# Kernel tuning notes

Hardware: AMD Instinct MI355X
Metric: run time of the kernel (lower is better)

## Reference

```python
import jax, jax.numpy as jnp
import numpy as np

D = 1024      # model_dim (input_dim)
H = 2048      # hidden_size_per_expert (hardcoded in module)
E = 8         # num_experts
K = 2         # topk
T = 8192      # tokens (batch after view)


def setup_inputs() -> dict:
    key = jax.random.key(0)
    ks = jax.random.split(key, 6)
    s_in = 1.0 / np.sqrt(D)
    s_h = 1.0 / np.sqrt(H)
    return {
        "x": jax.random.normal(ks[0], (T, D), dtype=jnp.float32),
        "wg": jax.random.normal(ks[1], (D, E), dtype=jnp.float32) * s_in,   # gate Linear(D,E,bias=False)
        "w1": jax.random.normal(ks[2], (E, D, H), dtype=jnp.float32) * s_in,
        "b1": jnp.zeros((E, H), dtype=jnp.float32),
        "w2": jax.random.normal(ks[3], (E, H, D), dtype=jnp.float32) * s_h,
        "b2": jnp.zeros((E, D), dtype=jnp.float32),
    }


def _moe(x, wg, w1, b1, w2, b2):
    # top-k gating (Tutel 'top' gate, k=K)
    logits = x @ wg                         # [T,E]
    scores = jax.nn.softmax(logits, -1)     # [T,E]
    topv, topi = jax.lax.top_k(scores, K)   # [T,K]
    sel = jax.nn.one_hot(topi, E, dtype=x.dtype)          # [T,K,E]
    combine = jnp.einsum('tk,tke->te', topv, sel)          # sparse combine weights [T,E]
    # GShard-style load-balance aux loss (top-1 dispatch mask)
    ce = sel[:, 0, :].mean(0)               # fraction of tokens whose top1 is e
    me = scores.mean(0)                     # mean gate prob per expert
    l_aux = jnp.sum(me * ce) * E
    # expert FFN (dense over experts; combine zeros out non-selected)
    h = jax.nn.relu(jnp.einsum('td,edh->teh', x, w1) + b1)  # [T,E,H]
    y = jnp.einsum('teh,ehd->ted', h, w2) + b2              # [T,E,D]
    out = jnp.einsum('te,ted->td', combine, y)              # [T,D]
    return out, l_aux


def reference(x, wg, w1, b1, w2, b2):
    return _moe(x, wg, w1, b1, w2, b2)
```

## Files before the change

kernel.cpp:

```cpp
#include <hip/hip_runtime.h>
#include <stdint.h>

#define T_TOK 8192
#define DIM   1024
#define HID   2048
#define NE    8

#define BM 256
#define BN 256
#define BK 64

#define GB_TOK 32

typedef float floatx4 __attribute__((ext_vector_type(4)));
typedef short shortx8 __attribute__((ext_vector_type(8)));

typedef __attribute__((address_space(3))) void       lds_void;
typedef const __attribute__((address_space(1))) void gbl_void;

__device__ __forceinline__ unsigned short f2bf(float f) {
  unsigned int u = __float_as_uint(f);
  unsigned int r = 0x7fffu + ((u >> 16) & 1u);
  return (unsigned short)((u + r) >> 16);
}

__global__ __launch_bounds__(256) void transpose_cast_kernel(const float* __restrict__ in,
                                                             unsigned short* __restrict__ out,
                                                             int R, int C) {
  __shared__ float tile[32][33];
  const size_t eoff = (size_t)blockIdx.z * R * C;
  const float* ip = in + eoff;
  unsigned short* op = out + eoff;
  int c0 = blockIdx.x * 32, r0 = blockIdx.y * 32;
  int tx = threadIdx.x, ty = threadIdx.y;
#pragma unroll
  for (int i = 0; i < 4; i++)
    tile[ty + i * 8][tx] = ip[(size_t)(r0 + ty + i * 8) * C + (c0 + tx)];
  __syncthreads();
#pragma unroll
  for (int i = 0; i < 4; i++)
    op[(size_t)(c0 + ty + i * 8) * R + (r0 + tx)] = f2bf(tile[tx][ty + i * 8]);
}

__global__ __launch_bounds__(256) void gate_kernel(const float* __restrict__ x,
                                                   const float* __restrict__ wg,
                                                   unsigned short* __restrict__ xb,
                                                   int* counts, int* top1cnt, float* ssum,
                                                   int* tok_list, float* wgt_list) {
  __shared__ int   lds_cnt[8];
  __shared__ int   lds_top1[8];
  __shared__ float lds_ssum[4][8];
  __shared__ int   tk_e[GB_TOK][2];
  __shared__ int   tk_r[GB_TOK][2];
  __shared__ float tk_w[GB_TOK][2];
  __shared__ int   base[8];

  const int tid = threadIdx.x;
  const int wave = tid >> 6;
  const int lane = tid & 63;

  if (tid < 8) { lds_cnt[tid] = 0; lds_top1[tid] = 0; }
  if (tid < 32) lds_ssum[tid >> 3][tid & 7] = 0.f;
  __syncthreads();

  float ssum_local[8];
#pragma unroll
  for (int e = 0; e < 8; e++) ssum_local[e] = 0.f;

  for (int it = 0; it < GB_TOK / 4; it++) {
    const int lt = it * 4 + wave;
    const int t = blockIdx.x * GB_TOK + lt;

    float acc[8];
#pragma unroll
    for (int e = 0; e < 8; e++) acc[e] = 0.f;
    const float* xr = x + (size_t)t * DIM;
    unsigned short* xw = xb + (size_t)t * DIM;
#pragma unroll
    for (int i = 0; i < 16; i++) {
      int d = i * 64 + lane;
      float xv = xr[d];
      xw[d] = f2bf(xv);
      const float4* wr = reinterpret_cast<const float4*>(wg + d * 8);
      float4 w0 = wr[0], w1 = wr[1];
      acc[0] += xv * w0.x; acc[1] += xv * w0.y; acc[2] += xv * w0.z; acc[3] += xv * w0.w;
      acc[4] += xv * w1.x; acc[5] += xv * w1.y; acc[6] += xv * w1.z; acc[7] += xv * w1.w;
    }
#pragma unroll
    for (int e = 0; e < 8; e++) {
#pragma unroll
      for (int off = 32; off > 0; off >>= 1) acc[e] += __shfl_xor(acc[e], off, 64);
    }
    if (lane == 0) {
      float mx = acc[0];
#pragma unroll
      for (int e = 1; e < 8; e++) mx = fmaxf(mx, acc[e]);
      float s[8], sum = 0.f;
#pragma unroll
      for (int e = 0; e < 8; e++) { s[e] = expf(acc[e] - mx); sum += s[e]; }
      float inv = 1.f / sum;
#pragma unroll
      for (int e = 0; e < 8; e++) { s[e] *= inv; ssum_local[e] += s[e]; }
      int i1 = 0;
#pragma unroll
      for (int e = 1; e < 8; e++) if (s[e] > s[i1]) i1 = e;
      int i2 = (i1 == 0) ? 1 : 0;
#pragma unroll
      for (int e = 0; e < 8; e++) if (e != i1 && s[e] > s[i2]) i2 = e;
      atomicAdd(&lds_top1[i1], 1);
      int r1 = atomicAdd(&lds_cnt[i1], 1);
      int r2 = atomicAdd(&lds_cnt[i2], 1);
      tk_e[lt][0] = i1; tk_r[lt][0] = r1; tk_w[lt][0] = s[i1];
      tk_e[lt][1] = i2; tk_r[lt][1] = r2; tk_w[lt][1] = s[i2];
    }
  }
  if (lane == 0) {
#pragma unroll
    for (int e = 0; e < 8; e++) lds_ssum[wave][e] = ssum_local[e];
  }
  __syncthreads();
  if (tid < 8) {
    base[tid] = atomicAdd(&counts[tid], lds_cnt[tid]);
    atomicAdd(&top1cnt[tid], lds_top1[tid]);
    atomicAdd(&ssum[tid],
              lds_ssum[0][tid] + lds_ssum[1][tid] + lds_ssum[2][tid] + lds_ssum[3][tid]);
  }
  __syncthreads();
  if (tid < GB_TOK * 2) {
    int lt = tid >> 1, k = tid & 1;
    int e = tk_e[lt][k];
    int pos = base[e] + tk_r[lt][k];
    tok_list[e * T_TOK + pos] = blockIdx.x * GB_TOK + lt;
    wgt_list[e * T_TOK + pos] = tk_w[lt][k];
  }
}

__global__ void scan_kernel(const int* counts, const int* top1cnt, const float* ssum,
                            int* h_off, float* laux_out) {
  if (threadIdx.x == 0 && blockIdx.x == 0) {
    int off = 0;
    float l = 0.f;
    for (int e = 0; e < 8; e++) {
      h_off[e] = off;
      off += counts[e];
      l += (ssum[e] / (float)T_TOK) * ((float)top1cnt[e] / (float)T_TOK);
    }
    *laux_out = l * (float)NE;
  }
}

template <int MODE>
__global__ __launch_bounds__(512, 2) void moe_gemm_kernel(
    const unsigned short* __restrict__ A_src, const unsigned short* __restrict__ B_src,
    const float* __restrict__ bias, const int* __restrict__ counts,
    const int* __restrict__ h_off, const int* __restrict__ tok_list,
    const float* __restrict__ wgt_list, unsigned short* __restrict__ h_out,
    float* __restrict__ out, int N, int K) {
  __shared__ unsigned short s_a[2][BM][BK];
  __shared__ unsigned short s_b[2][BN][BK];

  const int e = blockIdx.z;
  const int n_e = counts[e];
  const int m0 = blockIdx.y * BM;
  if (m0 >= n_e) return;
  const int n0 = blockIdx.x * BN;
  const int tid = threadIdx.x;

  const int lane = tid & 63;
  const int wv = tid >> 6;
  const int lrow = lane >> 3;
  const int lchk = (lane & 7) ^ lrow;

  const unsigned short* a_g[4];
  const unsigned short* b_g[4];
#pragma unroll
  for (int c = 0; c < 4; c++) {
    int ra = c * 64 + wv * 8 + lrow;
    int gr = m0 + ra;
    int safe = (gr < n_e) ? gr : (n_e - 1);
    const unsigned short* abase;
    if (MODE == 0) {
      int tok = tok_list[e * T_TOK + safe];
      abase = A_src + (size_t)tok * K;
    } else {
      abase = A_src + (size_t)(h_off[e] + safe) * K;
    }
    a_g[c] = abase + lchk * 8;
    b_g[c] = B_src + ((size_t)e * N + n0 + ra) * K + lchk * 8;
  }

  auto STAGE = [&](int buf, int kt) {
#pragma unroll
    for (int c = 0; c < 4; c++) {
      __builtin_amdgcn_global_load_lds((gbl_void*)(a_g[c] + kt),
                                       (lds_void*)&s_a[buf][c * 64 + wv * 8][0], 16, 0, 0);
      __builtin_amdgcn_global_load_lds((gbl_void*)(b_g[c] + kt),
                                       (lds_void*)&s_b[buf][c * 64 + wv * 8][0], 16, 0, 0);
    }
  };

  const int lm = lane & 15;
  const int quad = lane >> 4;
  const int r7 = lm & 7;
  const int wm = (wv >> 2) * 128;
  const int wn = (wv & 3) * 64;

  floatx4 acc[8][4];
#pragma unroll
  for (int mi = 0; mi < 8; mi++)
#pragma unroll
    for (int ni = 0; ni < 4; ni++) acc[mi][ni] = (floatx4){0.f, 0.f, 0.f, 0.f};

  const int NT = K / BK;
  STAGE(0, 0);
  __syncthreads();

  int cur = 0;
  for (int t = 0; t < NT; ++t) {
    if (t + 1 < NT) STAGE(cur ^ 1, (t + 1) * BK);
#pragma unroll
    for (int kk = 0; kk < 2; kk++) {
      const int pc = ((kk << 2) + quad) ^ r7;
      shortx8 af[8], bfr[4];
#pragma unroll
      for (int mi = 0; mi < 8; mi++)
        af[mi] = *reinterpret_cast<const shortx8*>(&s_a[cur][wm + mi * 16 + lm][pc << 3]);
#pragma unroll
      for (int ni = 0; ni < 4; ni++)
        bfr[ni] = *reinterpret_cast<const shortx8*>(&s_b[cur][wn + ni * 16 + lm][pc << 3]);
#pragma unroll
      for (int mi = 0; mi < 8; mi++)
#pragma unroll
        for (int ni = 0; ni < 4; ni++)
          acc[mi][ni] = __builtin_amdgcn_mfma_f32_16x16x32_bf16(af[mi], bfr[ni], acc[mi][ni], 0, 0, 0);
    }
    __syncthreads();
    cur ^= 1;
  }

#pragma unroll
  for (int mi = 0; mi < 8; mi++) {
#pragma unroll
    for (int r = 0; r < 4; r++) {
      int row = m0 + wm + mi * 16 + quad * 4 + r;
      if (row >= n_e) continue;
      if (MODE == 0) {
        size_t base = (size_t)(h_off[e] + row) * N;
#pragma unroll
        for (int ni = 0; ni < 4; ni++) {
          int col = n0 + wn + ni * 16 + lm;
          float v = acc[mi][ni][r] + bias[e * N + col];
          v = fmaxf(v, 0.f);
          h_out[base + col] = f2bf(v);
        }
      } else {
        int tok = tok_list[e * T_TOK + row];
        float wgt = wgt_list[e * T_TOK + row];
        size_t base = (size_t)tok * N;
#pragma unroll
        for (int ni = 0; ni < 4; ni++) {
          int col = n0 + wn + ni * 16 + lm;
          float v = wgt * (acc[mi][ni][r] + bias[e * N + col]);
          atomicAdd(&out[base + col], v);
        }
      }
    }
  }
}

extern "C" void kernel_launch(void* const* d_in, const int* in_sizes, int n_in,
                              void* d_out, int out_size, void* d_ws, size_t ws_size,
                              hipStream_t stream) {
  const float* x  = (const float*)d_in[0];
  const float* wg = (const float*)d_in[1];
  const float* w1 = (const float*)d_in[2];
  const float* b1 = (const float*)d_in[3];
  const float* w2 = (const float*)d_in[4];
  const float* b2 = (const float*)d_in[5];
  float* out = (float*)d_out;

  char* ws = (char*)d_ws;
  int*            counts   = (int*)(ws + 0);
  int*            top1cnt  = (int*)(ws + 32);
  float*          ssum     = (float*)(ws + 64);
  int*            h_off    = (int*)(ws + 96);
  int*            tok_list = (int*)(ws + 256);
  float*          wgt_list = (float*)(ws + 262400);
  unsigned short* x_bf     = (unsigned short*)(ws + 524544);
  unsigned short* w1t      = (unsigned short*)(ws + 17301760);
  unsigned short* w2t      = (unsigned short*)(ws + 50856192);
  unsigned short* h_buf    = (unsigned short*)(ws + 84410624);

  hipMemsetAsync(ws, 0, 256, stream);
  hipMemsetAsync(d_out, 0, (size_t)out_size * sizeof(float), stream);

  dim3 tb(32, 8);
  transpose_cast_kernel<<<dim3(HID / 32, DIM / 32, NE), tb, 0, stream>>>(w1, w1t, DIM, HID);
  transpose_cast_kernel<<<dim3(DIM / 32, HID / 32, NE), tb, 0, stream>>>(w2, w2t, HID, DIM);

  gate_kernel<<<T_TOK / GB_TOK, 256, 0, stream>>>(x, wg, x_bf, counts, top1cnt, ssum,
                                                  tok_list, wgt_list);
  scan_kernel<<<1, 64, 0, stream>>>(counts, top1cnt, ssum, h_off, out + (size_t)T_TOK * DIM);

  moe_gemm_kernel<0><<<dim3(HID / BN, T_TOK / BM, NE), 512, 0, stream>>>(
      x_bf, w1t, b1, counts, h_off, tok_list, wgt_list, h_buf, nullptr, HID, DIM);
  moe_gemm_kernel<1><<<dim3(DIM / BN, T_TOK / BM, NE), 512, 0, stream>>>(
      h_buf, w2t, b2, counts, h_off, tok_list, wgt_list, nullptr, out, DIM, HID);
}
```

Measured before the change: 574.0 us.

## Compact expert tile grid and software-pipeline MoE GEMM with split-K LDS stages

Replaces the per-expert 3D grid, which launched many empty blocks, with a compact 1D tile index built from prefix offsets computed in the scan kernel, so only real tiles are launched (at most 72). The GEMM main loop is rewritten as an explicit 8-phase pipeline: the LDS tile is split into two 32-wide K halves and two 128-row halves, and global-to-LDS loads are interleaved with MFMA groups using fine-grained barriers, vmcnt waits and setprio. A new XOR swizzle layout is used for the LDS reads. This trades simpler code for hand-scheduled synchronisation that depends on exact vmcnt accounting, and the fixed grid size of 72 assumes the tile count never exceeds it.

```diff
diff --git a/kernel.cpp b/kernel.cpp
--- a/kernel.cpp
+++ b/kernel.cpp
@@ -136,74 +136,125 @@
 }
 
 __global__ void scan_kernel(const int* counts, const int* top1cnt, const float* ssum,
-                            int* h_off, float* laux_out) {
+                            int* h_off, int* tile_off, float* laux_out) {
   if (threadIdx.x == 0 && blockIdx.x == 0) {
-    int off = 0;
+    int off = 0, toff = 0;
     float l = 0.f;
     for (int e = 0; e < 8; e++) {
       h_off[e] = off;
+      tile_off[e] = toff;
       off += counts[e];
+      toff += (counts[e] + BM - 1) / BM;
       l += (ssum[e] / (float)T_TOK) * ((float)top1cnt[e] / (float)T_TOK);
     }
+    tile_off[8] = toff;
     *laux_out = l * (float)NE;
   }
 }
+
+
+#define LDA4(buf, kk, mh)                                                        \
+  do {                                                                           \
+    const char* ha_ = (const char*)&s_a[buf][kk][0][0];                          \
+    _Pragma("unroll") for (int j_ = 0; j_ < 4; j_++)                             \
+        af[j_] = *reinterpret_cast<const shortx8*>(ha_ + aoff + ((mh)*4 + j_) * 1024); \
+  } while (0)
+
+#define LDB4(buf, kk)                                                            \
+  do {                                                                           \
+    const char* hb_ = (const char*)&s_b[buf][kk][0][0];                          \
+    _Pragma("unroll") for (int j_ = 0; j_ < 4; j_++)                             \
+        bfr[j_] = *reinterpret_cast<const shortx8*>(hb_ + boff + j_ * 1024);     \
+  } while (0)
+
+#define MFMA16(mh)                                                               \
+  do {                                                                           \
+    __builtin_amdgcn_s_setprio(1);                                               \
+    _Pragma("unroll") for (int j_ = 0; j_ < 4; j_++)                             \
+        _Pragma("unroll") for (int n_ = 0; n_ < 4; n_++)                         \
+            acc[(mh)*4 + j_][n_] = __builtin_amdgcn_mfma_f32_16x16x32_bf16(      \
+                af[j_], bfr[n_], acc[(mh)*4 + j_][n_], 0, 0, 0);                 \
+    __builtin_amdgcn_s_setprio(0);                                               \
+  } while (0)
+
+#define STAGE_A(buf, kk, tile)                                                   \
+  do {                                                                           \
+    __builtin_amdgcn_global_load_lds((gbl_void*)(a_p0 + (size_t)(tile)*64 + (kk)*32), \
+                                     (lds_void*)&s_a[buf][kk][wv * 8][0], 16, 0, 0);  \
+    __builtin_amdgcn_global_load_lds((gbl_void*)(a_p1 + (size_t)(tile)*64 + (kk)*32), \
+                                     (lds_void*)&s_a[buf][kk][64 + wv * 8][0], 16, 0, 0); \
+  } while (0)
+
+#define STAGE_B(buf, kk, tile)                                                   \
+  do {                                                                           \
+    __builtin_amdgcn_global_load_lds((gbl_void*)(b_p0 + (size_t)(tile)*64 + (kk)*32), \
+                                     (lds_void*)&s_b[buf][kk][wv * 8][0], 16, 0, 0);  \
+    __builtin_amdgcn_global_load_lds((gbl_void*)(b_p1 + (size_t)(tile)*64 + (kk)*32), \
+                                     (lds_void*)&s_b[buf][kk][64 + wv * 8][0], 16, 0, 0); \
+  } while (0)
+
+#define BAR()                                                                    \
+  do { __builtin_amdgcn_s_barrier(); asm volatile("" ::: "memory"); } while (0)
+#define BARW()                                                                   \
+  do {                                                                           \
+    __builtin_amdgcn_s_barrier();                                                \
+    asm volatile("s_waitcnt lgkmcnt(0)" ::: "memory");                           \
+  } while (0)
+#define VM4() asm volatile("s_waitcnt vmcnt(4)" ::: "memory")
 
 template <int MODE>
 __global__ __launch_bounds__(512, 2) void moe_gemm_kernel(
     const unsigned short* __restrict__ A_src, const unsigned short* __restrict__ B_src,
     const float* __restrict__ bias, const int* __restrict__ counts,
-    const int* __restrict__ h_off, const int* __restrict__ tok_list,
-    const float* __restrict__ wgt_list, unsigned short* __restrict__ h_out,
-    float* __restrict__ out, int N, int K) {
-  __shared__ unsigned short s_a[2][BM][BK];
-  __shared__ unsigned short s_b[2][BN][BK];
-
-  const int e = blockIdx.z;
+    const int* __restrict__ h_off, const int* __restrict__ tile_off,
+    const int* __restrict__ tok_list, const float* __restrict__ wgt_list,
+    unsigned short* __restrict__ h_out, float* __restrict__ out, int N, int K) {
+  __shared__ unsigned short s_a[2][2][128][64];
+  __shared__ unsigned short s_b[2][2][128][64];
+
+  const int bt = blockIdx.y;
+  if (bt >= tile_off[8]) return;
+  int e = 7;
+#pragma unroll
+  for (int q = 6; q >= 0; q--)
+    if (bt < tile_off[q + 1]) e = q;
   const int n_e = counts[e];
-  const int m0 = blockIdx.y * BM;
-  if (m0 >= n_e) return;
+  const int m0 = (bt - tile_off[e]) * BM;
   const int n0 = blockIdx.x * BN;
   const int tid = threadIdx.x;
 
   const int lane = tid & 63;
   const int wv = tid >> 6;
-  const int lrow = lane >> 3;
-  const int lchk = (lane & 7) ^ lrow;
-
-  const unsigned short* a_g[4];
-  const unsigned short* b_g[4];
-#pragma unroll
-  for (int c = 0; c < 4; c++) {
-    int ra = c * 64 + wv * 8 + lrow;
-    int gr = m0 + ra;
-    int safe = (gr < n_e) ? gr : (n_e - 1);
-    const unsigned short* abase;
+
+  const int slot = tid & 7;
+  const int Lr = tid >> 3;
+  const int g = slot ^ (Lr & 7);
+  const int rbase = 2 * Lr + (g >> 2);
+  const int cc8 = (g & 3) * 8;
+
+  const unsigned short *a_p0, *a_p1, *b_p0, *b_p1;
+  {
+    int gr0 = m0 + rbase, gr1 = m0 + 128 + rbase;
+    int s0 = (gr0 < n_e) ? gr0 : (n_e - 1);
+    int s1 = (gr1 < n_e) ? gr1 : (n_e - 1);
     if (MODE == 0) {
-      int tok = tok_list[e * T_TOK + safe];
-      abase = A_src + (size_t)tok * K;
+      a_p0 = A_src + (size_t)tok_list[e * T_TOK + s0] * K + cc8;
+      a_p1 = A_src + (size_t)tok_list[e * T_TOK + s1] * K + cc8;
     } else {
-      abase = A_src + (size_t)(h_off[e] + safe) * K;
-    }
-    a_g[c] = abase + lchk * 8;
-    b_g[c] = B_src + ((size_t)e * N + n0 + ra) * K + lchk * 8;
-  }
-
-  auto STAGE = [&](int buf, int kt) {
-#pragma unroll
-    for (int c = 0; c < 4; c++) {
-      __builtin_amdgcn_global_load_lds((gbl_void*)(a_g[c] + kt),
-                                       (lds_void*)&s_a[buf][c * 64 + wv * 8][0], 16, 0, 0);
-      __builtin_amdgcn_global_load_lds((gbl_void*)(b_g[c] + kt),
-                                       (lds_void*)&s_b[buf][c * 64 + wv * 8][0], 16, 0, 0);
-    }
-  };
+      a_p0 = A_src + (size_t)(h_off[e] + s0) * K + cc8;
+      a_p1 = A_src + (size_t)(h_off[e] + s1) * K + cc8;
+    }
+    b_p0 = B_src + ((size_t)e * N + n0 + rbase) * K + cc8;
+    b_p1 = B_src + ((size_t)e * N + n0 + 128 + rbase) * K + cc8;
+  }
 
   const int lm = lane & 15;
   const int quad = lane >> 4;
-  const int r7 = lm & 7;
   const int wm = (wv >> 2) * 128;
   const int wn = (wv & 3) * 64;
+  const int phys = (((lm & 1) << 2) | quad) ^ (lm >> 1);
+  const int aoff = (((wm >> 1) + (lm >> 1)) << 7) + (phys << 4);
+  const int boff = (((wn >> 1) + (lm >> 1)) << 7) + (phys << 4);
 
   floatx4 acc[8][4];
 #pragma unroll
@@ -212,31 +263,30 @@
     for (int ni = 0; ni < 4; ni++) acc[mi][ni] = (floatx4){0.f, 0.f, 0.f, 0.f};
 
   const int NT = K / BK;
-  STAGE(0, 0);
-  __syncthreads();
-
-  int cur = 0;
-  for (int t = 0; t < NT; ++t) {
-    if (t + 1 < NT) STAGE(cur ^ 1, (t + 1) * BK);
-#pragma unroll
-    for (int kk = 0; kk < 2; kk++) {
-      const int pc = ((kk << 2) + quad) ^ r7;
-      shortx8 af[8], bfr[4];
-#pragma unroll
-      for (int mi = 0; mi < 8; mi++)
-        af[mi] = *reinterpret_cast<const shortx8*>(&s_a[cur][wm + mi * 16 + lm][pc << 3]);
-#pragma unroll
-      for (int ni = 0; ni < 4; ni++)
-        bfr[ni] = *reinterpret_cast<const shortx8*>(&s_b[cur][wn + ni * 16 + lm][pc << 3]);
-#pragma unroll
-      for (int mi = 0; mi < 8; mi++)
-#pragma unroll
-        for (int ni = 0; ni < 4; ni++)
-          acc[mi][ni] = __builtin_amdgcn_mfma_f32_16x16x32_bf16(af[mi], bfr[ni], acc[mi][ni], 0, 0, 0);
-    }
-    __syncthreads();
-    cur ^= 1;
-  }
+  const int NI = NT / 2;
+
+  STAGE_A(0, 0, 0); STAGE_B(0, 0, 0);
+  STAGE_A(0, 1, 0); STAGE_B(0, 1, 0);
+  STAGE_A(1, 0, 1); STAGE_B(1, 0, 1);
+  asm volatile("s_waitcnt vmcnt(4)" ::: "memory");
+  BAR();
+
+  for (int i = 0; i < NI; ++i) {
+    const int tb = 2 * i + 1;
+    const int a2 = (2 * i + 2 < NT) ? (2 * i + 2) : (NT - 1);
+    const int b2 = (2 * i + 3 < NT) ? (2 * i + 3) : (NT - 1);
+    shortx8 af[4], bfr[4];
+    LDA4(0, 0, 0); LDB4(0, 0); STAGE_A(1, 1, tb);        BARW(); MFMA16(0); BAR();
+    LDA4(0, 0, 1);             STAGE_B(1, 1, tb);        BARW(); MFMA16(1); BAR();
+    LDA4(0, 1, 0); LDB4(0, 1); STAGE_A(0, 0, a2);        BARW(); MFMA16(0); BAR();
+    LDA4(0, 1, 1);             STAGE_B(0, 0, a2); VM4(); BARW(); MFMA16(1); BAR();
+    LDA4(1, 0, 0); LDB4(1, 0); STAGE_A(0, 1, a2);        BARW(); MFMA16(0); BAR();
+    LDA4(1, 0, 1);             STAGE_B(0, 1, a2);        BARW(); MFMA16(1); BAR();
+    LDA4(1, 1, 0); LDB4(1, 1); STAGE_A(1, 0, b2);        BARW(); MFMA16(0); BAR();
+    LDA4(1, 1, 1);             STAGE_B(1, 0, b2); VM4(); BARW(); MFMA16(1); BAR();
+  }
+
+  asm volatile("s_waitcnt vmcnt(0)" ::: "memory");
 
 #pragma unroll
   for (int mi = 0; mi < 8; mi++) {
@@ -284,6 +334,7 @@
   int*            top1cnt  = (int*)(ws + 32);
   float*          ssum     = (float*)(ws + 64);
   int*            h_off    = (int*)(ws + 96);
+  int*            tile_off = (int*)(ws + 128);
   int*            tok_list = (int*)(ws + 256);
   float*          wgt_list = (float*)(ws + 262400);
   unsigned short* x_bf     = (unsigned short*)(ws + 524544);
@@ -300,10 +351,11 @@
 
   gate_kernel<<<T_TOK / GB_TOK, 256, 0, stream>>>(x, wg, x_bf, counts, top1cnt, ssum,
                                                   tok_list, wgt_list);
-  scan_kernel<<<1, 64, 0, stream>>>(counts, top1cnt, ssum, h_off, out + (size_t)T_TOK * DIM);
-
-  moe_gemm_kernel<0><<<dim3(HID / BN, T_TOK / BM, NE), 512, 0, stream>>>(
-      x_bf, w1t, b1, counts, h_off, tok_list, wgt_list, h_buf, nullptr, HID, DIM);
-  moe_gemm_kernel<1><<<dim3(DIM / BN, T_TOK / BM, NE), 512, 0, stream>>>(
-      h_buf, w2t, b2, counts, h_off, tok_list, wgt_list, nullptr, out, DIM, HID);
-}
+  scan_kernel<<<1, 64, 0, stream>>>(counts, top1cnt, ssum, h_off, tile_off,
+                                    out + (size_t)T_TOK * DIM);
+
+  moe_gemm_kernel<0><<<dim3(HID / BN, 72, 1), 512, 0, stream>>>(
+      x_bf, w1t, b1, counts, h_off, tile_off, tok_list, wgt_list, h_buf, nullptr, HID, DIM);
+  moe_gemm_kernel<1><<<dim3(DIM / BN, 72, 1), 512, 0, stream>>>(
+      h_buf, w2t, b2, counts, h_off, tile_off, tok_list, wgt_list, nullptr, out, DIM, HID);
+}
```

Measured after the change: 538.2 us. -6.2%, faster.

## Use compact per-expert tile schedule with smaller 128x128 GEMM tiles

Applied to the files above, without the earlier changes.

Replaces the dense (N-tile, max-M-tile, expert) grid with a flat list of M-tiles computed by prefix sums over per-expert token counts. Each block finds its expert by searching tile_off, so no blocks launch only to exit. Tiles shrink from 256x256 with 512 threads to 128x128 with 256 threads. This is meant to cut empty blocks and raise CU occupancy and load balance, at the cost of less operand reuse per tile and more global/LDS traffic per FLOP. The grid height of 136 is fixed as an upper bound on the tile count (8192*2/128 + 8).

```diff
diff --git a/kernel.cpp b/kernel.cpp
--- a/kernel.cpp
+++ b/kernel.cpp
@@ -6,8 +6,8 @@
 #define HID   2048
 #define NE    8
 
-#define BM 256
-#define BN 256
+#define BM 128
+#define BN 128
 #define BK 64
 
 #define GB_TOK 32
@@ -136,33 +136,40 @@
 }
 
 __global__ void scan_kernel(const int* counts, const int* top1cnt, const float* ssum,
-                            int* h_off, float* laux_out) {
+                            int* h_off, int* tile_off, float* laux_out) {
   if (threadIdx.x == 0 && blockIdx.x == 0) {
-    int off = 0;
+    int off = 0, toff = 0;
     float l = 0.f;
     for (int e = 0; e < 8; e++) {
       h_off[e] = off;
+      tile_off[e] = toff;
       off += counts[e];
+      toff += (counts[e] + BM - 1) / BM;
       l += (ssum[e] / (float)T_TOK) * ((float)top1cnt[e] / (float)T_TOK);
     }
+    tile_off[8] = toff;
     *laux_out = l * (float)NE;
   }
 }
 
 template <int MODE>
-__global__ __launch_bounds__(512, 2) void moe_gemm_kernel(
+__global__ __launch_bounds__(256, 2) void moe_gemm_kernel(
     const unsigned short* __restrict__ A_src, const unsigned short* __restrict__ B_src,
     const float* __restrict__ bias, const int* __restrict__ counts,
-    const int* __restrict__ h_off, const int* __restrict__ tok_list,
-    const float* __restrict__ wgt_list, unsigned short* __restrict__ h_out,
-    float* __restrict__ out, int N, int K) {
+    const int* __restrict__ h_off, const int* __restrict__ tile_off,
+    const int* __restrict__ tok_list, const float* __restrict__ wgt_list,
+    unsigned short* __restrict__ h_out, float* __restrict__ out, int N, int K) {
   __shared__ unsigned short s_a[2][BM][BK];
   __shared__ unsigned short s_b[2][BN][BK];
 
-  const int e = blockIdx.z;
+  const int bt = blockIdx.y;
+  if (bt >= tile_off[8]) return;
+  int e = 7;
+#pragma unroll
+  for (int q = 6; q >= 0; q--)
+    if (bt < tile_off[q + 1]) e = q;
   const int n_e = counts[e];
-  const int m0 = blockIdx.y * BM;
-  if (m0 >= n_e) return;
+  const int m0 = (bt - tile_off[e]) * BM;
   const int n0 = blockIdx.x * BN;
   const int tid = threadIdx.x;
 
@@ -175,7 +182,7 @@
   const unsigned short* b_g[4];
 #pragma unroll
   for (int c = 0; c < 4; c++) {
-    int ra = c * 64 + wv * 8 + lrow;
+    int ra = wv * 32 + c * 8 + lrow;
     int gr = m0 + ra;
     int safe = (gr < n_e) ? gr : (n_e - 1);
     const unsigned short* abase;
@@ -193,21 +200,21 @@
 #pragma unroll
     for (int c = 0; c < 4; c++) {
       __builtin_amdgcn_global_load_lds((gbl_void*)(a_g[c] + kt),
-                                       (lds_void*)&s_a[buf][c * 64 + wv * 8][0], 16, 0, 0);
+                                       (lds_void*)&s_a[buf][wv * 32 + c * 8][0], 16, 0, 0);
       __builtin_amdgcn_global_load_lds((gbl_void*)(b_g[c] + kt),
-                                       (lds_void*)&s_b[buf][c * 64 + wv * 8][0], 16, 0, 0);
+                                       (lds_void*)&s_b[buf][wv * 32 + c * 8][0], 16, 0, 0);
     }
   };
 
   const int lm = lane & 15;
   const int quad = lane >> 4;
   const int r7 = lm & 7;
-  const int wm = (wv >> 2) * 128;
-  const int wn = (wv & 3) * 64;
-
-  floatx4 acc[8][4];
-#pragma unroll
-  for (int mi = 0; mi < 8; mi++)
+  const int wm = (wv >> 1) * 64;
+  const int wn = (wv & 1) * 64;
+
+  floatx4 acc[4][4];
+#pragma unroll
+  for (int mi = 0; mi < 4; mi++)
 #pragma unroll
     for (int ni = 0; ni < 4; ni++) acc[mi][ni] = (floatx4){0.f, 0.f, 0.f, 0.f};
 
@@ -221,15 +228,15 @@
 #pragma unroll
     for (int kk = 0; kk < 2; kk++) {
       const int pc = ((kk << 2) + quad) ^ r7;
-      shortx8 af[8], bfr[4];
-#pragma unroll
-      for (int mi = 0; mi < 8; mi++)
+      shortx8 af[4], bfr[4];
+#pragma unroll
+      for (int mi = 0; mi < 4; mi++)
         af[mi] = *reinterpret_cast<const shortx8*>(&s_a[cur][wm + mi * 16 + lm][pc << 3]);
 #pragma unroll
       for (int ni = 0; ni < 4; ni++)
         bfr[ni] = *reinterpret_cast<const shortx8*>(&s_b[cur][wn + ni * 16 + lm][pc << 3]);
 #pragma unroll
-      for (int mi = 0; mi < 8; mi++)
+      for (int mi = 0; mi < 4; mi++)
 #pragma unroll
         for (int ni = 0; ni < 4; ni++)
           acc[mi][ni] = __builtin_amdgcn_mfma_f32_16x16x32_bf16(af[mi], bfr[ni], acc[mi][ni], 0, 0, 0);
@@ -239,7 +246,7 @@
   }
 
 #pragma unroll
-  for (int mi = 0; mi < 8; mi++) {
+  for (int mi = 0; mi < 4; mi++) {
 #pragma unroll
     for (int r = 0; r < 4; r++) {
       int row = m0 + wm + mi * 16 + quad * 4 + r;
@@ -284,6 +291,7 @@
   int*            top1cnt  = (int*)(ws + 32);
   float*          ssum     = (float*)(ws + 64);
   int*            h_off    = (int*)(ws + 96);
+  int*            tile_off = (int*)(ws + 128);
   int*            tok_list = (int*)(ws + 256);
   float*          wgt_list = (float*)(ws + 262400);
   unsigned short* x_bf     = (unsigned short*)(ws + 524544);
@@ -300,10 +308,11 @@
 
   gate_kernel<<<T_TOK / GB_TOK, 256, 0, stream>>>(x, wg, x_bf, counts, top1cnt, ssum,
                                                   tok_list, wgt_list);
-  scan_kernel<<<1, 64, 0, stream>>>(counts, top1cnt, ssum, h_off, out + (size_t)T_TOK * DIM);
-
-  moe_gemm_kernel<0><<<dim3(HID / BN, T_TOK / BM, NE), 512, 0, stream>>>(
-      x_bf, w1t, b1, counts, h_off, tok_list, wgt_list, h_buf, nullptr, HID, DIM);
-  moe_gemm_kernel<1><<<dim3(DIM / BN, T_TOK / BM, NE), 512, 0, stream>>>(
-      h_buf, w2t, b2, counts, h_off, tok_list, wgt_list, nullptr, out, DIM, HID);
-}
+  scan_kernel<<<1, 64, 0, stream>>>(counts, top1cnt, ssum, h_off, tile_off,
+                                    out + (size_t)T_TOK * DIM);
+
+  moe_gemm_kernel<0><<<dim3(HID / BN, 136, 1), 256, 0, stream>>>(
+      x_bf, w1t, b1, counts, h_off, tile_off, tok_list, wgt_list, h_buf, nullptr, HID, DIM);
+  moe_gemm_kernel<1><<<dim3(DIM / BN, 136, 1), 256, 0, stream>>>(
+      h_buf, w2t, b2, counts, h_off, tile_off, tok_list, wgt_list, nullptr, out, DIM, HID);
+}
```

Result: faster. 539.9 us (-5.9%).
